# Optimization experiments

Hardware: AMD Instinct MI355X
Metric: run time of the kernel (lower is better)

The kernel has to match this reference:

```python
import jax, jax.numpy as jnp
import numpy as np

T = 5
V_TH = 0.5
GAMMA = 0.5
W_DECAY = 0.5
LOWER = 0.2 - 0.03
UPPER = 0.2 + 0.03
EMA_INIT = 0.17

@jax.custom_vjp
def sg_heaviside(x):
    return (x >= 0).astype(x.dtype)

def _sg_fwd(x):
    return sg_heaviside(x), x

def _sg_bwd(x, g):
    # grad_output * clamp(gamma - |x|, 0) / gamma^2  (triangular surrogate)
    return (g * jnp.clip(GAMMA - jnp.abs(x), 0.0) / (GAMMA * GAMMA),)

sg_heaviside.defvjp(_sg_fwd, _sg_bwd)


def setup_inputs() -> dict:
    key = jax.random.key(0)
    k1, k2 = jax.random.split(key)
    shape = (T, 32, 128, 32, 32)  # [T, B, C, H, W]
    x_exc = jax.random.uniform(k1, shape, dtype=jnp.float32)
    x_inh = jax.random.uniform(k2, shape, dtype=jnp.float32)
    alpha_raw = jnp.zeros((), dtype=jnp.float32)  # nn.Parameter alpha init 0.0
    beta_raw = jnp.zeros((), dtype=jnp.float32)   # nn.Parameter beta init 0.0
    return {"x_exc": x_exc, "x_inh": x_inh, "alpha_raw": alpha_raw, "beta_raw": beta_raw}


def reference(x_exc, x_inh, alpha_raw, beta_raw):
    beta = jax.nn.sigmoid(beta_raw)
    alpha = 4.0 * jax.nn.sigmoid(alpha_raw)
    B, C, H, W = x_exc.shape[1:]
    mem0 = jnp.zeros((B, C, H, W), x_exc.dtype)
    # ema starts constant 0.17 full-shape; after first mean it is [1,C,1,1].
    # Starting with [1,C,1,1] constant is mathematically identical.
    ema0 = jnp.full((1, C, 1, 1), EMA_INIT, x_exc.dtype)
    inhw0 = jnp.zeros((1, C, 1, 1), x_exc.dtype)

    def step(carry, xs):
        mem, ema, inhw = carry
        xe, xi = xs
        e_input = xe / (1.0 + alpha * xi)
        mem = W_DECAY * mem + e_input - beta * xi * (1.0 - inhw)
        spike = sg_heaviside(mem - V_TH)
        # ema update uses detached spikes; broadcasts [1,C,1,1]+[B,C,H,W] then means back
        ema = jnp.mean(0.9 * ema + 0.1 * jax.lax.stop_gradient(spike),
                       axis=(0, 2, 3), keepdims=True)
        # original only updates inh_weight for t < T-1, but the last update is
        # never read, so updating unconditionally is equivalent
        inhw = 4.0 * (jax.nn.sigmoid(LOWER - ema) - jax.nn.sigmoid(ema - UPPER))
        mem = mem - V_TH * spike
        return (mem, ema, inhw), spike

    _, spikes = jax.lax.scan(step, (mem0, ema0, inhw0), (x_exc, x_inh))
    return spikes  # [T, B, C, H, W]
```

## Files before the change

kernel.cpp:

```cpp
#include <hip/hip_runtime.h>
#include <hip/hip_cooperative_groups.h>

namespace cg = cooperative_groups;

constexpr int T    = 5;
constexpr int C    = 128;
constexpr int NPT4 = 32 * C * 1024 / 4;

constexpr int SBLOCKS  = 1024;
constexpr int STHREADS = 256;
constexpr int KT       = 4;

constexpr size_t PART_BYTES = (size_t)T * SBLOCKS * sizeof(unsigned int);
constexpr size_t WS_NEEDED  = PART_BYTES + (size_t)NPT4 * 16;

__global__ __launch_bounds__(STHREADS, 4)
void lif_coop(const float4* __restrict__ xe4,
              const float4* __restrict__ xi4,
              const float* __restrict__ alpha_raw,
              const float* __restrict__ beta_raw,
              float4* __restrict__ out4,
              unsigned int* __restrict__ partials) {
#pragma clang fp contract(off)
  const int blk = blockIdx.x;
  const int tid = threadIdx.x;
  const int c   = blk & (C - 1);
  __shared__ float s_inhw;
  __shared__ unsigned int wsum[STHREADS / 64];

  const float alpha = 4.0f / (1.0f + expf(-alpha_raw[0]));
  const float beta  = 1.0f / (1.0f + expf(-beta_raw[0]));

  const size_t fi0 = (size_t)blk * 256 + tid;

  float4 e[KT], i[KT], en[KT], ix[KT];
#pragma unroll
  for (int k = 0; k < KT; ++k) {
    const size_t fi = fi0 + (size_t)(k * SBLOCKS) * 256;
    e[k] = xe4[fi];
    i[k] = xi4[fi];
  }

  float mv[KT][4];
#pragma unroll
  for (int k = 0; k < KT; ++k)
#pragma unroll
    for (int j = 0; j < 4; ++j) mv[k][j] = 0.0f;

  float inhw = 0.0f;
  float ema  = 0.17f;
  cg::grid_group grid = cg::this_grid();

  for (int t = 0; t < T; ++t) {
    const size_t tb = (size_t)t * NPT4;

    if (t < T - 1) {
      const size_t tb1 = tb + NPT4;
#pragma unroll
      for (int k = 0; k < KT; ++k) {
        const size_t fi = fi0 + (size_t)(k * SBLOCKS) * 256;
        en[k] = xe4[tb1 + fi];
        ix[k] = xi4[tb1 + fi];
      }
    }

    unsigned int local = 0;
#pragma unroll
    for (int k = 0; k < KT; ++k) {
      const size_t fi = fi0 + (size_t)(k * SBLOCKS) * 256;
      const float xe[4] = {e[k].x, e[k].y, e[k].z, e[k].w};
      const float xi[4] = {i[k].x, i[k].y, i[k].z, i[k].w};
      float sv[4];
#pragma unroll
      for (int j = 0; j < 4; ++j) {
        const float e_in = xe[j] / (1.0f + alpha * xi[j]);
        const float a  = 0.5f * mv[k][j];
        const float bb = a + e_in;
        const float d  = (beta * xi[j]) * (1.0f - inhw);
        const float m  = bb - d;
        const float x  = m - 0.5f;
        const float s  = (x >= 0.0f) ? 1.0f : 0.0f;
        local += (x >= 0.0f) ? 1u : 0u;
        mv[k][j] = m - 0.5f * s;
        sv[j] = s;
      }
      float4 s4; s4.x = sv[0]; s4.y = sv[1]; s4.z = sv[2]; s4.w = sv[3];
      out4[tb + fi] = s4;
    }
    if (t == T - 1) break;

#pragma unroll
    for (int off = 32; off > 0; off >>= 1) local += __shfl_down(local, off);
    if ((tid & 63) == 0) wsum[tid >> 6] = local;
    __syncthreads();
    if (tid == 0) {
      const unsigned int total = wsum[0] + wsum[1] + wsum[2] + wsum[3];
      __hip_atomic_store(&partials[t * SBLOCKS + blk], total,
                         __ATOMIC_RELEASE, __HIP_MEMORY_SCOPE_AGENT);
    }

    grid.sync();

    if (tid == 0) {
      unsigned int tot = 0;
#pragma unroll
      for (int q = 0; q < 8; ++q)
        tot += __hip_atomic_load(&partials[t * SBLOCKS + c + q * C],
                                 __ATOMIC_ACQUIRE, __HIP_MEMORY_SCOPE_AGENT);
      const float mean = (float)tot * (1.0f / 32768.0f);
      ema = 0.9f * ema + 0.1f * mean;
      const float s_lo = 1.0f / (1.0f + expf(-(0.17f - ema)));
      const float s_hi = 1.0f / (1.0f + expf(-(ema - 0.23f)));
      s_inhw = 4.0f * (s_lo - s_hi);
    }
    __syncthreads();
    inhw = s_inhw;

#pragma unroll
    for (int k = 0; k < KT; ++k) { e[k] = en[k]; i[k] = ix[k]; }
  }
}

__global__ __launch_bounds__(STHREADS)
void lif_step(const float4* __restrict__ xe4,
              const float4* __restrict__ xi4,
              const float* __restrict__ alpha_raw,
              const float* __restrict__ beta_raw,
              float4* __restrict__ out4,
              float4* __restrict__ memb,
              unsigned int* __restrict__ partials,
              int t) {
#pragma clang fp contract(off)
  const int blk = blockIdx.x;
  const int tid = threadIdx.x;
  const int c   = blk & (C - 1);

  __shared__ float s_inhw;
  if (tid == 0) {
    float inhw = 0.0f;
    if (t > 0) {
      float ema = 0.17f;
      for (int s = 0; s < t; ++s) {
        unsigned int tot = 0;
#pragma unroll
        for (int i = 0; i < 8; ++i) tot += partials[s * SBLOCKS + c + i * C];
        const float mean = (float)tot * (1.0f / 32768.0f);
        ema = 0.9f * ema + 0.1f * mean;
      }
      const float s_lo = 1.0f / (1.0f + expf(-(0.17f - ema)));
      const float s_hi = 1.0f / (1.0f + expf(-(ema - 0.23f)));
      inhw = 4.0f * (s_lo - s_hi);
    }
    s_inhw = inhw;
  }
  __syncthreads();
  const float inhw  = s_inhw;
  const float alpha = 4.0f / (1.0f + expf(-alpha_raw[0]));
  const float beta  = 1.0f / (1.0f + expf(-beta_raw[0]));

  unsigned int local = 0;
  const size_t tb = (size_t)t * NPT4;
#pragma unroll
  for (int k = 0; k < KT; ++k) {
    const size_t fi = (size_t)(k * SBLOCKS + blk) * 256 + tid;
    const float4 e4 = xe4[tb + fi];
    const float4 i4 = xi4[tb + fi];
    float4 m4 = {0.0f, 0.0f, 0.0f, 0.0f};
    if (t > 0) m4 = memb[fi];
    const float xe[4] = {e4.x, e4.y, e4.z, e4.w};
    const float xi[4] = {i4.x, i4.y, i4.z, i4.w};
    float mv[4] = {m4.x, m4.y, m4.z, m4.w};
    float sv[4];
#pragma unroll
    for (int j = 0; j < 4; ++j) {
      const float e_in = xe[j] / (1.0f + alpha * xi[j]);
      const float a  = 0.5f * mv[j];
      const float bb = a + e_in;
      const float d  = (beta * xi[j]) * (1.0f - inhw);
      const float m  = bb - d;
      const float x  = m - 0.5f;
      const float s  = (x >= 0.0f) ? 1.0f : 0.0f;
      local += (x >= 0.0f) ? 1u : 0u;
      mv[j] = m - 0.5f * s;
      sv[j] = s;
    }
    float4 s4; s4.x = sv[0]; s4.y = sv[1]; s4.z = sv[2]; s4.w = sv[3];
    out4[tb + fi] = s4;
    if (t < T - 1) {
      float4 nm; nm.x = mv[0]; nm.y = mv[1]; nm.z = mv[2]; nm.w = mv[3];
      memb[fi] = nm;
    }
  }

  if (t < T - 1) {
#pragma unroll
    for (int off = 32; off > 0; off >>= 1) local += __shfl_down(local, off);
    __shared__ unsigned int wsum[STHREADS / 64];
    if ((tid & 63) == 0) wsum[tid >> 6] = local;
    __syncthreads();
    if (tid == 0)
      partials[t * SBLOCKS + blk] = wsum[0] + wsum[1] + wsum[2] + wsum[3];
  }
}

constexpr int FTHREADS = 1024;
constexpr int FWAVES   = FTHREADS / 64;
constexpr int FBLOCKS  = 2 * C;
constexpr int FK       = 8;

__global__ __launch_bounds__(FTHREADS)
void lif_fallback(const float* __restrict__ xe_g, const float* __restrict__ xi_g,
                  const float* __restrict__ alpha_raw,
                  const float* __restrict__ beta_raw, float* __restrict__ out) {
#pragma clang fp contract(off)
  const int blk = blockIdx.x, c = blk & (C - 1), half = blk >> 7;
  const int tid = threadIdx.x, wave = tid >> 6, lane = tid & 63;
  __shared__ unsigned int wsum[T - 1][FWAVES];
  const float alpha = 4.0f / (1.0f + expf(-alpha_raw[0]));
  const float beta  = 1.0f / (1.0f + expf(-beta_raw[0]));
  float mem[FK][4];
#pragma unroll
  for (int k = 0; k < FK; ++k)
#pragma unroll
    for (int j = 0; j < 4; ++j) mem[k][j] = 0.0f;
  float ema = 0.17f, inhw = 0.0f;
  const float4* xe4 = (const float4*)xe_g;
  const float4* xi4 = (const float4*)xi_g;
  float4* o4 = (float4*)out;
  auto gidx = [&](int t, int k) -> size_t {
    const int b = k * (FTHREADS / 256) + (tid >> 8);
    return (size_t)t * NPT4 + (size_t)(b * C + c) * 256 + (tid & 255);
  };
  for (int t = 0; t < T; ++t) {
    float4 e4[FK], i4[FK];
#pragma unroll
    for (int k = 0; k < FK; ++k) { const size_t idx = gidx(t, k); e4[k] = xe4[idx]; i4[k] = xi4[idx]; }
    unsigned int local = 0;
#pragma unroll
    for (int k = 0; k < FK; ++k) {
      const float xe[4] = {e4[k].x, e4[k].y, e4[k].z, e4[k].w};
      const float xi[4] = {i4[k].x, i4[k].y, i4[k].z, i4[k].w};
      float sv[4];
#pragma unroll
      for (int j = 0; j < 4; ++j) {
        const float e_in = xe[j] / (1.0f + alpha * xi[j]);
        const float a = 0.5f * mem[k][j];
        const float bb = a + e_in;
        const float d = (beta * xi[j]) * (1.0f - inhw);
        const float m = bb - d;
        const float x = m - 0.5f;
        const float s = (x >= 0.0f) ? 1.0f : 0.0f;
        local += (x >= 0.0f) ? 1u : 0u;
        mem[k][j] = m - 0.5f * s;
        sv[j] = s;
      }
      if ((k >> 2) == half) {
        float4 s4; s4.x = sv[0]; s4.y = sv[1]; s4.z = sv[2]; s4.w = sv[3];
        o4[gidx(t, k)] = s4;
      }
    }
    if (t == T - 1) break;
#pragma unroll
    for (int off = 32; off > 0; off >>= 1) local += __shfl_down(local, off);
    if (lane == 0) wsum[t][wave] = local;
    __syncthreads();
    unsigned int total = 0;
#pragma unroll
    for (int w = 0; w < FWAVES; ++w) total += wsum[t][w];
    const float mean_spike = (float)total * (1.0f / 32768.0f);
    ema = 0.9f * ema + 0.1f * mean_spike;
    const float s_lo = 1.0f / (1.0f + expf(-(0.17f - ema)));
    const float s_hi = 1.0f / (1.0f + expf(-(ema - 0.23f)));
    inhw = 4.0f * (s_lo - s_hi);
  }
}

extern "C" void kernel_launch(void* const* d_in, const int* in_sizes, int n_in,
                              void* d_out, int out_size, void* d_ws, size_t ws_size,
                              hipStream_t stream) {
  const float* xe = (const float*)d_in[0];
  const float* xi = (const float*)d_in[1];
  const float* ar = (const float*)d_in[2];
  const float* br = (const float*)d_in[3];
  float* out = (float*)d_out;

  static const int coop_ok = [] {
    int dev = 0;
    if (hipGetDevice(&dev) != hipSuccess) return 0;
    int attr = 0;
    if (hipDeviceGetAttribute(&attr, hipDeviceAttributeCooperativeLaunch, dev) != hipSuccess || !attr)
      return 0;
    int nb = 0;
    if (hipOccupancyMaxActiveBlocksPerMultiprocessor(&nb, (const void*)lif_coop,
                                                     STHREADS, 0) != hipSuccess)
      return 0;
    int cus = 0;
    if (hipDeviceGetAttribute(&cus, hipDeviceAttributeMultiprocessorCount, dev) != hipSuccess)
      return 0;
    return (nb * cus >= SBLOCKS) ? 1 : 0;
  }();

  if (coop_ok && ws_size >= PART_BYTES) {
    unsigned int* partials = (unsigned int*)d_ws;
    const float4* xe4 = (const float4*)xe;
    const float4* xi4 = (const float4*)xi;
    float4* out4 = (float4*)out;
    void* args[6];
    args[0] = (void*)&xe4;
    args[1] = (void*)&xi4;
    args[2] = (void*)&ar;
    args[3] = (void*)&br;
    args[4] = (void*)&out4;
    args[5] = (void*)&partials;
    (void)hipLaunchCooperativeKernel((const void*)lif_coop, dim3(SBLOCKS),
                                     dim3(STHREADS), args, 0, stream);
  } else if (ws_size >= WS_NEEDED) {
    unsigned int* partials = (unsigned int*)d_ws;
    float4* memb = (float4*)((char*)d_ws + PART_BYTES);
    const float4* xe4 = (const float4*)xe;
    const float4* xi4 = (const float4*)xi;
    float4* out4 = (float4*)out;
    for (int t = 0; t < T; ++t)
      lif_step<<<dim3(SBLOCKS), dim3(STHREADS), 0, stream>>>(
          xe4, xi4, ar, br, out4, memb, partials, t);
  } else {
    lif_fallback<<<dim3(FBLOCKS), dim3(FTHREADS), 0, stream>>>(xe, xi, ar, br, out);
  }
}
```

Measured before the change: 226.9 us.

## Replace cooperative grid sync with per-channel atomic counters and spin-wait

Drops the cooperative launch and its grid-wide barrier. Each block now atomically adds its spike count, with an arrival tag in the top bits, into a per-channel, per-timestep cell, then spins until all 8 blocks of that channel have arrived. This means blocks wait only on their 8 channel peers instead of the whole grid, at the cost of a memset launch before the kernel. Correctness depends on all 1024 blocks being co-resident, which is checked only via occupancy and not guaranteed by a cooperative launch.

Result: no change. 230.5 us (+1.6%).

```diff
diff --git a/kernel.cpp b/kernel.cpp
--- a/kernel.cpp
+++ b/kernel.cpp
@@ -1,7 +1,4 @@
 #include <hip/hip_runtime.h>
-#include <hip/hip_cooperative_groups.h>
-
-namespace cg = cooperative_groups;
 
 constexpr int T    = 5;
 constexpr int C    = 128;
@@ -11,16 +8,17 @@
 constexpr int STHREADS = 256;
 constexpr int KT       = 4;
 
+constexpr size_t ACC_BYTES  = (size_t)T * C * sizeof(unsigned int);
 constexpr size_t PART_BYTES = (size_t)T * SBLOCKS * sizeof(unsigned int);
-constexpr size_t WS_NEEDED  = PART_BYTES + (size_t)NPT4 * 16;
+constexpr size_t WS_R8      = PART_BYTES + (size_t)NPT4 * 16;
 
 __global__ __launch_bounds__(STHREADS, 4)
-void lif_coop(const float4* __restrict__ xe4,
-              const float4* __restrict__ xi4,
-              const float* __restrict__ alpha_raw,
-              const float* __restrict__ beta_raw,
-              float4* __restrict__ out4,
-              unsigned int* __restrict__ partials) {
+void lif_stream(const float4* __restrict__ xe4,
+                const float4* __restrict__ xi4,
+                const float* __restrict__ alpha_raw,
+                const float* __restrict__ beta_raw,
+                float4* __restrict__ out4,
+                unsigned int* __restrict__ acc) {
 #pragma clang fp contract(off)
   const int blk = blockIdx.x;
   const int tid = threadIdx.x;
@@ -49,7 +47,6 @@
 
   float inhw = 0.0f;
   float ema  = 0.17f;
-  cg::grid_group grid = cg::this_grid();
 
   for (int t = 0; t < T; ++t) {
     const size_t tb = (size_t)t * NPT4;
@@ -95,18 +92,16 @@
     __syncthreads();
     if (tid == 0) {
       const unsigned int total = wsum[0] + wsum[1] + wsum[2] + wsum[3];
-      __hip_atomic_store(&partials[t * SBLOCKS + blk], total,
-                         __ATOMIC_RELEASE, __HIP_MEMORY_SCOPE_AGENT);
-    }
-
-    grid.sync();
-
-    if (tid == 0) {
-      unsigned int tot = 0;
-#pragma unroll
-      for (int q = 0; q < 8; ++q)
-        tot += __hip_atomic_load(&partials[t * SBLOCKS + c + q * C],
-                                 __ATOMIC_ACQUIRE, __HIP_MEMORY_SCOPE_AGENT);
+      unsigned int* cell = &acc[t * C + c];
+      __hip_atomic_fetch_add(cell, total | (1u << 28),
+                             __ATOMIC_RELEASE, __HIP_MEMORY_SCOPE_AGENT);
+      unsigned int v = __hip_atomic_load(cell, __ATOMIC_ACQUIRE,
+                                         __HIP_MEMORY_SCOPE_AGENT);
+      while ((v >> 28) < 8u) {
+        __builtin_amdgcn_s_sleep(2);
+        v = __hip_atomic_load(cell, __ATOMIC_ACQUIRE, __HIP_MEMORY_SCOPE_AGENT);
+      }
+      const unsigned int tot = v & 0x0FFFFFFFu;
       const float mean = (float)tot * (1.0f / 32768.0f);
       ema = 0.9f * ema + 0.1f * mean;
       const float s_lo = 1.0f / (1.0f + expf(-(0.17f - ema)));
@@ -283,15 +278,15 @@
   const float* ar = (const float*)d_in[2];
   const float* br = (const float*)d_in[3];
   float* out = (float*)d_out;
-
-  static const int coop_ok = [] {
+  const float4* xe4 = (const float4*)xe;
+  const float4* xi4 = (const float4*)xi;
+  float4* out4 = (float4*)out;
+
+  static const int stream_ok = [] {
     int dev = 0;
     if (hipGetDevice(&dev) != hipSuccess) return 0;
-    int attr = 0;
-    if (hipDeviceGetAttribute(&attr, hipDeviceAttributeCooperativeLaunch, dev) != hipSuccess || !attr)
-      return 0;
     int nb = 0;
-    if (hipOccupancyMaxActiveBlocksPerMultiprocessor(&nb, (const void*)lif_coop,
+    if (hipOccupancyMaxActiveBlocksPerMultiprocessor(&nb, (const void*)lif_stream,
                                                      STHREADS, 0) != hipSuccess)
       return 0;
     int cus = 0;
@@ -300,26 +295,14 @@
     return (nb * cus >= SBLOCKS) ? 1 : 0;
   }();
 
-  if (coop_ok && ws_size >= PART_BYTES) {
-    unsigned int* partials = (unsigned int*)d_ws;
-    const float4* xe4 = (const float4*)xe;
-    const float4* xi4 = (const float4*)xi;
-    float4* out4 = (float4*)out;
-    void* args[6];
-    args[0] = (void*)&xe4;
-    args[1] = (void*)&xi4;
-    args[2] = (void*)&ar;
-    args[3] = (void*)&br;
-    args[4] = (void*)&out4;
-    args[5] = (void*)&partials;
-    (void)hipLaunchCooperativeKernel((const void*)lif_coop, dim3(SBLOCKS),
-                                     dim3(STHREADS), args, 0, stream);
-  } else if (ws_size >= WS_NEEDED) {
+  if (stream_ok && ws_size >= ACC_BYTES) {
+    unsigned int* acc = (unsigned int*)d_ws;
+    hipMemsetAsync(d_ws, 0, ACC_BYTES, stream);
+    lif_stream<<<dim3(SBLOCKS), dim3(STHREADS), 0, stream>>>(
+        xe4, xi4, ar, br, out4, acc);
+  } else if (ws_size >= WS_R8) {
     unsigned int* partials = (unsigned int*)d_ws;
     float4* memb = (float4*)((char*)d_ws + PART_BYTES);
-    const float4* xe4 = (const float4*)xe;
-    const float4* xi4 = (const float4*)xi;
-    float4* out4 = (float4*)out;
     for (int t = 0; t < T; ++t)
       lif_step<<<dim3(SBLOCKS), dim3(STHREADS), 0, stream>>>(
           xe4, xi4, ar, br, out4, memb, partials, t);
```
